# Kernel optimization log

Hardware: AMD Instinct MI355X
Metric: run time of the kernel (lower is better)

## Reference

```python
import jax, jax.numpy as jnp
import numpy as np

N, E = 100000, 1600000
IN_DIM, HID, NCLS = 64, 128, 18
BATCH, K = 8, 5000


def setup_inputs() -> dict:
    key = jax.random.key(0)
    ks = jax.random.split(key, 9)
    features = jax.random.normal(ks[0], (N, IN_DIM), dtype=jnp.float32)
    src = jax.random.randint(ks[1], (E,), 0, N, dtype=jnp.int32)
    dst = jax.random.randint(ks[2], (E,), 0, N, dtype=jnp.int32)
    def glorot(k, shape):
        lim = float(np.sqrt(6.0 / (shape[0] + shape[1])))
        return jax.random.uniform(k, shape, jnp.float32, -lim, lim)
    W1 = glorot(ks[3], (IN_DIM, HID)); b1 = jnp.zeros((HID,), jnp.float32)
    W2 = glorot(ks[4], (HID, HID));    b2 = jnp.zeros((HID,), jnp.float32)
    W3 = glorot(ks[5], (K * HID, NCLS)); b3 = jnp.zeros((NCLS,), jnp.float32)
    return {"features": features, "src": src, "dst": dst,
            "W1": W1, "b1": b1, "W2": W2, "b2": b2, "W3": W3, "b3": b3}


def reference(features, src, dst, W1, b1, W2, b2, W3, b3):
    n = features.shape[0]
    ones = jnp.ones(src.shape[0], features.dtype)
    out_deg = jax.ops.segment_sum(ones, src, num_segments=n)
    in_deg = jax.ops.segment_sum(ones, dst, num_segments=n)
    norm_src = jnp.clip(out_deg, 1.0) ** -0.5  # DGL norm='both'
    norm_dst = jnp.clip(in_deg, 1.0) ** -0.5

    def gconv(x, W, b, act):
        h = (x @ W) * norm_src[:, None]          # transform then normalize src
        agg = jax.ops.segment_sum(h[src], dst, num_segments=n)  # gather+scatter-add
        agg = agg * norm_dst[:, None] + b
        return jax.nn.relu(agg) if act else agg

    h = gconv(features, W1, b1, True)   # [N, HID]
    h = gconv(h, W2, b2, True)          # [N, HID]

    # global_sort_pool: equal-sized graphs of N//BATCH nodes, top-K by last channel
    n_per = n // BATCH
    hb = h.reshape(BATCH, n_per, HID)
    _, idx = jax.lax.top_k(hb[..., -1], K)                  # [B, K] descending
    topk = jnp.take_along_axis(hb, idx[..., None], axis=1)  # [B, K, HID]
    pooled = topk.reshape(BATCH, K * HID)

    return pooled @ W3 + b3  # [B, NCLS]
```

## Files before the change

### kernel.cpp

```cpp
#include <hip/hip_runtime.h>
#include <cstdint>
#include <cstddef>

#define N_NODES 100000
#define N_EDGES 1600000
#define IN_DIM  64
#define HID     128
#define NCLS    18
#define BATCH   8
#define TOPK    5000
#define NPER    12500
#define SORTN   16384
#define SORTC   2048

#define BSHIFT  9
#define BNODES  (1 << BSHIFT)
#define NBUCK   ((N_NODES + BNODES - 1) / BNODES)
#define CHUNK   8192


__global__ __launch_bounds__(256) void k_bcount(const int* __restrict__ src,
                                                const int* __restrict__ dst,
                                                int* __restrict__ bcntS,
                                                int* __restrict__ bcntD) {
    __shared__ int cs[NBUCK], cd[NBUCK];
    for (int b = threadIdx.x; b < NBUCK; b += 256) { cs[b] = 0; cd[b] = 0; }
    __syncthreads();
    const int base = blockIdx.x * CHUNK;
    const int end  = min(base + CHUNK, N_EDGES);
    for (int e = base + threadIdx.x; e < end; e += 256) {
        atomicAdd(&cs[src[e] >> BSHIFT], 1);
        atomicAdd(&cd[dst[e] >> BSHIFT], 1);
    }
    __syncthreads();
    for (int b = threadIdx.x; b < NBUCK; b += 256) {
        if (cs[b]) atomicAdd(&bcntS[b], cs[b]);
        if (cd[b]) atomicAdd(&bcntD[b], cd[b]);
    }
}

__global__ void k_bscan(const int* __restrict__ bcntS, const int* __restrict__ bcntD,
                        int* __restrict__ baseS, int* __restrict__ baseD,
                        int* __restrict__ curS, int* __restrict__ curD) {
    if (threadIdx.x == 0 && blockIdx.x == 0) {
        int rs = 0, rd = 0;
        for (int b = 0; b < NBUCK; ++b) {
            baseS[b] = rs; curS[b] = rs; rs += bcntS[b];
            baseD[b] = rd; curD[b] = rd; rd += bcntD[b];
        }
        baseS[NBUCK] = rs; baseD[NBUCK] = rd;
    }
}


__global__ __launch_bounds__(256) void k_bin2(const int* __restrict__ src,
                                              const int* __restrict__ dst,
                                              int* __restrict__ cursorD,
                                              int* __restrict__ cursorS,
                                              unsigned* __restrict__ binbuf,
                                              unsigned* __restrict__ sbin) {
    __shared__ int cD[NBUCK], gD[NBUCK], aD[NBUCK];
    __shared__ int cS[NBUCK], gS[NBUCK], aS[NBUCK];
    const int base = blockIdx.x * CHUNK;
    const int end  = min(base + CHUNK, N_EDGES);
    for (int b = threadIdx.x; b < NBUCK; b += 256) {
        cD[b] = 0; aD[b] = 0; cS[b] = 0; aS[b] = 0;
    }
    __syncthreads();
    for (int e = base + threadIdx.x; e < end; e += 256) {
        atomicAdd(&cD[dst[e] >> BSHIFT], 1);
        atomicAdd(&cS[src[e] >> BSHIFT], 1);
    }
    __syncthreads();
    for (int b = threadIdx.x; b < NBUCK; b += 256) {
        if (cD[b] > 0) gD[b] = atomicAdd(&cursorD[b], cD[b]);
        if (cS[b] > 0) gS[b] = atomicAdd(&cursorS[b], cS[b]);
    }
    __syncthreads();
    for (int e = base + threadIdx.x; e < end; e += 256) {
        int d = dst[e], s = src[e];
        int bd = d >> BSHIFT;
        int od = atomicAdd(&aD[bd], 1);
        binbuf[gD[bd] + od] = ((unsigned)(d & (BNODES - 1)) << 17) | (unsigned)s;
        int bs = s >> BSHIFT;
        int os = atomicAdd(&aS[bs], 1);
        sbin[gS[bs] + os] = (unsigned)(s & (BNODES - 1));
    }
}


__global__ __launch_bounds__(256) void k_hist_all(const unsigned* __restrict__ sbin,
                                                  const int* __restrict__ baseS,
                                                  const unsigned* __restrict__ binbuf,
                                                  const int* __restrict__ baseD,
                                                  float* __restrict__ normS,
                                                  float* __restrict__ normD,
                                                  int* __restrict__ row_ptr,
                                                  int* __restrict__ ssrc) {
    __shared__ int cnt[BNODES];
    __shared__ int tmp[BNODES];
    const int nodeBase = blockIdx.x << BSHIFT;
    for (int t = threadIdx.x; t < BNODES; t += 256) cnt[t] = 0;
    __syncthreads();
    {
        const int beg = baseS[blockIdx.x], end = baseS[blockIdx.x + 1];
        for (int e = beg + threadIdx.x; e < end; e += 256)
            atomicAdd(&cnt[sbin[e]], 1);
    }
    __syncthreads();
    for (int t = threadIdx.x; t < BNODES; t += 256) {
        int node = nodeBase + t;
        if (node < N_NODES)
            normS[node] = 1.0f / sqrtf((float)max(cnt[t], 1));
        cnt[t] = 0;
    }
    __syncthreads();
    const int beg = baseD[blockIdx.x], end = baseD[blockIdx.x + 1];
    for (int e = beg + threadIdx.x; e < end; e += 256)
        atomicAdd(&cnt[binbuf[e] >> 17], 1);
    __syncthreads();
    for (int t = threadIdx.x; t < BNODES; t += 256) {
        int node = nodeBase + t;
        if (node < N_NODES)
            normD[node] = 1.0f / sqrtf((float)max(cnt[t], 1));
    }
    for (int s = 1; s < BNODES; s <<= 1) {
        for (int t = threadIdx.x; t < BNODES; t += 256)
            tmp[t] = (t >= s) ? cnt[t - s] + cnt[t] : cnt[t];
        __syncthreads();
        for (int t = threadIdx.x; t < BNODES; t += 256) cnt[t] = tmp[t];
        __syncthreads();
    }
    for (int t = threadIdx.x; t < BNODES; t += 256) {
        int b = beg + ((t == 0) ? 0 : cnt[t - 1]);
        tmp[t] = b;
        int node = nodeBase + t;
        if (node < N_NODES) row_ptr[node] = b;
    }
    if (blockIdx.x == 0 && threadIdx.x == 0) row_ptr[N_NODES] = N_EDGES;
    __syncthreads();
    for (int e = beg + threadIdx.x; e < end; e += 256) {
        unsigned v = binbuf[e];
        int pos = atomicAdd(&tmp[v >> 17], 1);
        ssrc[pos] = (int)(v & 0x1FFFFu);
    }
}


#define BMT 64
#define BKT 32

__global__ __launch_bounds__(256) void k_fused1(const float* __restrict__ X,
                                                const int* __restrict__ row_ptr,
                                                const int* __restrict__ ssrc,
                                                const float* __restrict__ normS,
                                                const float* __restrict__ W,
                                                const float* __restrict__ normD,
                                                const float* __restrict__ bias,
                                                float* __restrict__ out) {
    __shared__ float xs[BMT][IN_DIM + 4];
    __shared__ float ws[BKT * HID];

    const int tid = threadIdx.x;
    const int rt = blockIdx.x * BMT;

    {
        constexpr int LPN = IN_DIM / 4;
        constexpr int NCH = 256 / LPN;
        const int w = tid / LPN;
        const int lane = tid % LPN;
        const float4* __restrict__ hv = (const float4*)X;
        #pragma unroll
        for (int c = 0; c < BMT / NCH; ++c) {
            const int row = c * NCH + w;
            const int node = rt + row;
            float4 a4 = make_float4(0.f, 0.f, 0.f, 0.f);
            if (node < N_NODES) {
                const int beg = row_ptr[node], end = row_ptr[node + 1];
                int e = beg;
                for (; e + 4 <= end; e += 4) {
                    int s0 = ssrc[e + 0], s1 = ssrc[e + 1], s2 = ssrc[e + 2], s3 = ssrc[e + 3];
                    float n0 = normS[s0], n1 = normS[s1], n2 = normS[s2], n3 = normS[s3];
                    float4 v0 = hv[(size_t)s0 * LPN + lane];
                    float4 v1 = hv[(size_t)s1 * LPN + lane];
                    float4 v2 = hv[(size_t)s2 * LPN + lane];
                    float4 v3 = hv[(size_t)s3 * LPN + lane];
                    a4.x += v0.x * n0; a4.y += v0.y * n0; a4.z += v0.z * n0; a4.w += v0.w * n0;
                    a4.x += v1.x * n1; a4.y += v1.y * n1; a4.z += v1.z * n1; a4.w += v1.w * n1;
                    a4.x += v2.x * n2; a4.y += v2.y * n2; a4.z += v2.z * n2; a4.w += v2.w * n2;
                    a4.x += v3.x * n3; a4.y += v3.y * n3; a4.z += v3.z * n3; a4.w += v3.w * n3;
                }
                for (; e < end; ++e) {
                    int s0 = ssrc[e];
                    float n0 = normS[s0];
                    float4 v0 = hv[(size_t)s0 * LPN + lane];
                    a4.x += v0.x * n0; a4.y += v0.y * n0; a4.z += v0.z * n0; a4.w += v0.w * n0;
                }
            }
            *(float4*)&xs[row][lane * 4] = a4;
        }
    }

    const int tx = tid & 31;
    const int ty = tid >> 5;
    const int col0 = tx * 4;
    const int row0 = ty * 8;

    float acc[8][4];
    #pragma unroll
    for (int r = 0; r < 8; ++r)
        #pragma unroll
        for (int c = 0; c < 4; ++c) acc[r][c] = 0.f;

    for (int k0 = 0; k0 < IN_DIM; k0 += BKT) {
        __syncthreads();
        {
            const float4* wsrc = (const float4*)(W + (size_t)k0 * HID);
            #pragma unroll
            for (int i = tid; i < BKT * HID / 4; i += 256)
                ((float4*)ws)[i] = wsrc[i];
        }
        __syncthreads();
        #pragma unroll 4
        for (int k = 0; k < BKT; ++k) {
            float4 b = *(const float4*)&ws[k * HID + col0];
            float a[8];
            #pragma unroll
            for (int r = 0; r < 8; ++r) a[r] = xs[row0 + r][k0 + k];
            #pragma unroll
            for (int r = 0; r < 8; ++r) {
                acc[r][0] += a[r] * b.x;
                acc[r][1] += a[r] * b.y;
                acc[r][2] += a[r] * b.z;
                acc[r][3] += a[r] * b.w;
            }
        }
    }

    const float4 bb = *(const float4*)(bias + col0);
    #pragma unroll
    for (int r = 0; r < 8; ++r) {
        int gr = rt + row0 + r;
        if (gr < N_NODES) {
            float nd = normD[gr];
            float4 o;
            o.x = fmaxf(acc[r][0] * nd + bb.x, 0.f);
            o.y = fmaxf(acc[r][1] * nd + bb.y, 0.f);
            o.z = fmaxf(acc[r][2] * nd + bb.z, 0.f);
            o.w = fmaxf(acc[r][3] * nd + bb.w, 0.f);
            float ns = normS[gr];
            o.x *= ns; o.y *= ns; o.z *= ns; o.w *= ns;
            *(float4*)(out + (size_t)gr * HID + col0) = o;
        }
    }
}


#define ACC4(A, V) { A.x += V.x; A.y += V.y; A.z += V.z; A.w += V.w; }

__global__ __launch_bounds__(256) void k_agg128(const float* __restrict__ hs,
                                                const int* __restrict__ row_ptr,
                                                const int* __restrict__ ssrc,
                                                float* __restrict__ out) {
    const int node = blockIdx.x * 8 + (threadIdx.x >> 5);
    const int lane = threadIdx.x & 31;
    if (node >= N_NODES) return;
    const int beg = row_ptr[node], end = row_ptr[node + 1];
    const float4* __restrict__ hv = (const float4*)hs;
    float4 acc = make_float4(0.f, 0.f, 0.f, 0.f);
    int e = beg;
    for (; e + 4 <= end; e += 4) {
        int s0 = ssrc[e + 0], s1 = ssrc[e + 1], s2 = ssrc[e + 2], s3 = ssrc[e + 3];
        float4 v0 = hv[(size_t)s0 * 32 + lane];
        float4 v1 = hv[(size_t)s1 * 32 + lane];
        float4 v2 = hv[(size_t)s2 * 32 + lane];
        float4 v3 = hv[(size_t)s3 * 32 + lane];
        ACC4(acc, v0); ACC4(acc, v1); ACC4(acc, v2); ACC4(acc, v3);
    }
    for (; e < end; ++e) {
        float4 v0 = hv[(size_t)ssrc[e] * 32 + lane];
        ACC4(acc, v0);
    }
    *(float4*)(out + (size_t)node * HID + lane * 4) = acc;
}


__global__ __launch_bounds__(256) void k_gemm2(const float* __restrict__ X,
                                               const float* __restrict__ W,
                                               const float* __restrict__ normD,
                                               const float* __restrict__ bias,
                                               float* __restrict__ keys,
                                               float* __restrict__ out) {
    __shared__ float xs[BMT][BKT + 4];
    __shared__ float ws[BKT * HID];

    const int tid = threadIdx.x;
    const int tx = tid & 31;
    const int ty = tid >> 5;
    const int col0 = tx * 4;
    const int row0 = ty * 8;
    const int rt = blockIdx.x * BMT;

    float acc[8][4];
    #pragma unroll
    for (int r = 0; r < 8; ++r)
        #pragma unroll
        for (int c = 0; c < 4; ++c) acc[r][c] = 0.f;

    for (int k0 = 0; k0 < HID; k0 += BKT) {
        __syncthreads();
        {
            const float4* wsrc = (const float4*)(W + (size_t)k0 * HID);
            #pragma unroll
            for (int i = tid; i < BKT * HID / 4; i += 256)
                ((float4*)ws)[i] = wsrc[i];
        }
        {
            #pragma unroll
            for (int i = tid; i < BMT * BKT / 4; i += 256) {
                int row = i >> 3;
                int kq  = i & 7;
                int gr  = rt + row;
                float4 v = make_float4(0.f, 0.f, 0.f, 0.f);
                if (gr < N_NODES)
                    v = *(const float4*)(X + (size_t)gr * HID + k0 + kq * 4);
                *(float4*)&xs[row][kq * 4] = v;
            }
        }
        __syncthreads();

        #pragma unroll 4
        for (int k = 0; k < BKT; ++k) {
            float4 b = *(const float4*)&ws[k * HID + col0];
            float a[8];
            #pragma unroll
            for (int r = 0; r < 8; ++r) a[r] = xs[row0 + r][k];
            #pragma unroll
            for (int r = 0; r < 8; ++r) {
                acc[r][0] += a[r] * b.x;
                acc[r][1] += a[r] * b.y;
                acc[r][2] += a[r] * b.z;
                acc[r][3] += a[r] * b.w;
            }
        }
    }

    const float4 bb = *(const float4*)(bias + col0);
    #pragma unroll
    for (int r = 0; r < 8; ++r) {
        int gr = rt + row0 + r;
        if (gr < N_NODES) {
            float nd = normD[gr];
            float4 o;
            o.x = fmaxf(acc[r][0] * nd + bb.x, 0.f);
            o.y = fmaxf(acc[r][1] * nd + bb.y, 0.f);
            o.z = fmaxf(acc[r][2] * nd + bb.z, 0.f);
            o.w = fmaxf(acc[r][3] * nd + bb.w, 0.f);
            if (col0 == 124) keys[gr] = o.w;
            *(float4*)(out + (size_t)gr * HID + col0) = o;
        }
    }
}


__global__ __launch_bounds__(256) void k_sort_init(const float* __restrict__ keys,
                                                   unsigned long long* __restrict__ arr) {
    int i = blockIdx.x * 256 + threadIdx.x;
    if (i >= BATCH * SORTN) return;
    int g = i >> 14;
    int l = i & (SORTN - 1);
    unsigned long long c;
    if (l < NPER) {
        unsigned u = __float_as_uint(keys[g * NPER + l]);
        unsigned s = (u & 0x80000000u) ? ~u : (u | 0x80000000u);
        unsigned d = ~s;
        c = ((unsigned long long)d << 32) | (unsigned)l;
    } else {
        c = 0xFFFFFFFFFFFFFFFFull;
    }
    arr[i] = c;
}

__global__ __launch_bounds__(1024) void k_sort_local_full(unsigned long long* __restrict__ arr) {
    __shared__ unsigned long long lds[SORTC];
    const int base  = blockIdx.x * SORTC;
    const int gbase = base & (SORTN - 1);
    lds[threadIdx.x]        = arr[base + threadIdx.x];
    lds[threadIdx.x + 1024] = arr[base + threadIdx.x + 1024];
    __syncthreads();
    for (int k = 2; k <= SORTC; k <<= 1) {
        for (int j = k >> 1; j > 0; j >>= 1) {
            int t = threadIdx.x;
            int i = ((t & ~(j - 1)) << 1) | (t & (j - 1));
            bool up = (((gbase + i) & k) == 0);
            unsigned long long a = lds[i], b = lds[i + j];
            if ((a > b) == up) { lds[i] = b; lds[i + j] = a; }
            __syncthreads();
        }
    }
    arr[base + threadIdx.x]        = lds[threadIdx.x];
    arr[base + threadIdx.x + 1024] = lds[threadIdx.x + 1024];
}

__global__ __launch_bounds__(256) void k_sort_global(unsigned long long* __restrict__ arr,
                                                     int k, int j) {
    int tg = blockIdx.x * 256 + threadIdx.x;
    if (tg >= BATCH * (SORTN / 2)) return;
    int g = tg >> 13;
    int t = tg & (SORTN / 2 - 1);
    int i = ((t & ~(j - 1)) << 1) | (t & (j - 1));
    bool up = ((i & k) == 0);
    unsigned long long* p = arr + (size_t)g * SORTN;
    unsigned long long a = p[i], b = p[i + j];
    if ((a > b) == up) { p[i] = b; p[i + j] = a; }
}

__global__ __launch_bounds__(1024) void k_sort_local_tail(unsigned long long* __restrict__ arr,
                                                          int k) {
    __shared__ unsigned long long lds[SORTC];
    const int base  = blockIdx.x * SORTC;
    const int gbase = base & (SORTN - 1);
    lds[threadIdx.x]        = arr[base + threadIdx.x];
    lds[threadIdx.x + 1024] = arr[base + threadIdx.x + 1024];
    __syncthreads();
    for (int j = SORTC >> 1; j > 0; j >>= 1) {
        int t = threadIdx.x;
        int i = ((t & ~(j - 1)) << 1) | (t & (j - 1));
        bool up = (((gbase + i) & k) == 0);
        unsigned long long a = lds[i], b = lds[i + j];
        if ((a > b) == up) { lds[i] = b; lds[i + j] = a; }
        __syncthreads();
    }
    arr[base + threadIdx.x]        = lds[threadIdx.x];
    arr[base + threadIdx.x + 1024] = lds[threadIdx.x + 1024];
}

__global__ __launch_bounds__(256) void k_sort_emit(const unsigned long long* __restrict__ arr,
                                                   int* __restrict__ topk_idx,
                                                   const float* __restrict__ b3,
                                                   float* __restrict__ out) {
    int i = blockIdx.x * 256 + threadIdx.x;
    if (i < BATCH * NCLS) out[i] = b3[i % NCLS];
    if (i >= BATCH * TOPK) return;
    int b = i / TOPK;
    int k = i - b * TOPK;
    topk_idx[i] = (int)(arr[(size_t)b * SORTN + k] & 0xFFFFFFFFull);
}


#define KPB 100

__global__ __launch_bounds__(128) void k_final(const float* __restrict__ h2,
                                               const int* __restrict__ topk_idx,
                                               const float* __restrict__ W3,
                                               float* __restrict__ out) {
    __shared__ float red[128 * NCLS];
    const int b = blockIdx.x / (TOPK / KPB);
    const int chunk = blockIdx.x % (TOPK / KPB);
    const int j = threadIdx.x;
    float acc[NCLS];
    #pragma unroll
    for (int c = 0; c < NCLS; ++c) acc[c] = 0.f;
    const int k0 = chunk * KPB;
    for (int k = k0; k < k0 + KPB; ++k) {
        int node = b * NPER + topk_idx[b * TOPK + k];
        float h = h2[(size_t)node * HID + j];
        const float* wrow = W3 + (size_t)(k * HID + j) * NCLS;
        #pragma unroll
        for (int c = 0; c < NCLS; ++c) acc[c] += h * wrow[c];
    }
    #pragma unroll
    for (int c = 0; c < NCLS; ++c) red[j * NCLS + c] = acc[c];
    __syncthreads();
    for (int s = 64; s > 0; s >>= 1) {
        if (j < s) {
            #pragma unroll
            for (int c = 0; c < NCLS; ++c) red[j * NCLS + c] += red[(j + s) * NCLS + c];
        }
        __syncthreads();
    }
    if (j < NCLS) atomicAdd(&out[b * NCLS + j], red[j]);
}


extern "C" void kernel_launch(void* const* d_in, const int* in_sizes, int n_in,
                              void* d_out, int out_size, void* d_ws, size_t ws_size,
                              hipStream_t stream) {
    const float* features = (const float*)d_in[0];
    const int*   src      = (const int*)d_in[1];
    const int*   dst      = (const int*)d_in[2];
    const float* W1       = (const float*)d_in[3];
    const float* b1       = (const float*)d_in[4];
    const float* W2       = (const float*)d_in[5];
    const float* b2       = (const float*)d_in[6];
    const float* W3       = (const float*)d_in[7];
    const float* b3       = (const float*)d_in[8];
    float* out = (float*)d_out;

    char* p = (char*)d_ws;
    auto carve = [&](size_t bytes) -> void* {
        void* r = (void*)p;
        p += (bytes + 511) & ~(size_t)511;
        return r;
    };
    float* normS     = (float*)carve((size_t)N_NODES * 4);
    float* normD     = (float*)carve((size_t)N_NODES * 4);
    int*   row_ptr   = (int*)carve((size_t)(N_NODES + 1) * 4);
    int*   bcntS     = (int*)carve((size_t)NBUCK * 4);
    int*   bcntD     = (int*)carve((size_t)NBUCK * 4);
    int*   baseS     = (int*)carve((size_t)(NBUCK + 1) * 4);
    int*   baseD     = (int*)carve((size_t)(NBUCK + 1) * 4);
    int*   curS      = (int*)carve((size_t)NBUCK * 4);
    int*   curD      = (int*)carve((size_t)NBUCK * 4);
    int*   ssrc      = (int*)carve((size_t)N_EDGES * 4);
    unsigned* binbuf = (unsigned*)carve((size_t)N_EDGES * 4);
    unsigned* sbin   = (unsigned*)carve((size_t)N_EDGES * 4);
    float* keys      = (float*)carve((size_t)N_NODES * 4);
    int*   topk_idx  = (int*)carve((size_t)BATCH * TOPK * 4);
    unsigned long long* sortbuf = (unsigned long long*)carve((size_t)BATCH * SORTN * 8);
    float* bufA      = (float*)carve((size_t)N_NODES * HID * 4);
    float* bufB      = (float*)carve((size_t)N_NODES * HID * 4);

    const int GB = (N_NODES + BMT - 1) / BMT;
    const int BB = (N_EDGES + CHUNK - 1) / CHUNK;

    hipMemsetAsync(bcntS, 0, (size_t)NBUCK * 4, stream);
    hipMemsetAsync(bcntD, 0, (size_t)NBUCK * 4, stream);

    k_bcount<<<BB, 256, 0, stream>>>(src, dst, bcntS, bcntD);
    k_bscan<<<1, 64, 0, stream>>>(bcntS, bcntD, baseS, baseD, curS, curD);
    k_bin2<<<BB, 256, 0, stream>>>(src, dst, curD, curS, binbuf, sbin);
    k_hist_all<<<NBUCK, 256, 0, stream>>>(sbin, baseS, binbuf, baseD,
                                          normS, normD, row_ptr, ssrc);

    k_fused1<<<GB, 256, 0, stream>>>(features, row_ptr, ssrc, normS, W1, normD, b1, bufA);
    k_agg128<<<(N_NODES + 7) / 8, 256, 0, stream>>>(bufA, row_ptr, ssrc, bufB);
    k_gemm2<<<GB, 256, 0, stream>>>(bufB, W2, normD, b2, keys, bufA);

    const int NCHUNK = BATCH * SORTN / SORTC;
    const int GCE    = (BATCH * (SORTN / 2) + 255) / 256;
    k_sort_init<<<(BATCH * SORTN + 255) / 256, 256, 0, stream>>>(keys, sortbuf);
    k_sort_local_full<<<NCHUNK, 1024, 0, stream>>>(sortbuf);
    k_sort_global<<<GCE, 256, 0, stream>>>(sortbuf, 4096, 2048);
    k_sort_local_tail<<<NCHUNK, 1024, 0, stream>>>(sortbuf, 4096);
    k_sort_global<<<GCE, 256, 0, stream>>>(sortbuf, 8192, 4096);
    k_sort_global<<<GCE, 256, 0, stream>>>(sortbuf, 8192, 2048);
    k_sort_local_tail<<<NCHUNK, 1024, 0, stream>>>(sortbuf, 8192);
    k_sort_global<<<GCE, 256, 0, stream>>>(sortbuf, 16384, 8192);
    k_sort_global<<<GCE, 256, 0, stream>>>(sortbuf, 16384, 4096);
    k_sort_global<<<GCE, 256, 0, stream>>>(sortbuf, 16384, 2048);
    k_sort_local_tail<<<NCHUNK, 1024, 0, stream>>>(sortbuf, 16384);
    k_sort_emit<<<(BATCH * TOPK + 255) / 256, 256, 0, stream>>>(sortbuf, topk_idx, b3, out);

    k_final<<<BATCH * (TOPK / KPB), 128, 0, stream>>>(bufA, topk_idx, W3, out);
}
```

Before: 578.4 us.

## Restructure bitonic top-k sort into fewer LDS-resident merge kernels

```diff
diff --git a/kernel.cpp b/kernel.cpp
--- a/kernel.cpp
+++ b/kernel.cpp
@@ -149,6 +149,7 @@
 
 #define BMT 64
 #define BKT 32
+#define BKT1 16
 
 __global__ __launch_bounds__(256) void k_fused1(const float* __restrict__ X,
                                                 const int* __restrict__ row_ptr,
@@ -159,7 +160,7 @@
                                                 const float* __restrict__ bias,
                                                 float* __restrict__ out) {
     __shared__ float xs[BMT][IN_DIM + 4];
-    __shared__ float ws[BKT * HID];
+    __shared__ float ws[BKT1 * HID];
 
     const int tid = threadIdx.x;
     const int rt = blockIdx.x * BMT;
@@ -212,17 +213,17 @@
         #pragma unroll
         for (int c = 0; c < 4; ++c) acc[r][c] = 0.f;
 
-    for (int k0 = 0; k0 < IN_DIM; k0 += BKT) {
+    for (int k0 = 0; k0 < IN_DIM; k0 += BKT1) {
         __syncthreads();
         {
             const float4* wsrc = (const float4*)(W + (size_t)k0 * HID);
             #pragma unroll
-            for (int i = tid; i < BKT * HID / 4; i += 256)
+            for (int i = tid; i < BKT1 * HID / 4; i += 256)
                 ((float4*)ws)[i] = wsrc[i];
         }
         __syncthreads();
         #pragma unroll 4
-        for (int k = 0; k < BKT; ++k) {
+        for (int k = 0; k < BKT1; ++k) {
             float4 b = *(const float4*)&ws[k * HID + col0];
             float a[8];
             #pragma unroll
@@ -363,30 +364,26 @@
 }
 
 
-__global__ __launch_bounds__(256) void k_sort_init(const float* __restrict__ keys,
-                                                   unsigned long long* __restrict__ arr) {
-    int i = blockIdx.x * 256 + threadIdx.x;
-    if (i >= BATCH * SORTN) return;
-    int g = i >> 14;
-    int l = i & (SORTN - 1);
-    unsigned long long c;
-    if (l < NPER) {
-        unsigned u = __float_as_uint(keys[g * NPER + l]);
-        unsigned s = (u & 0x80000000u) ? ~u : (u | 0x80000000u);
-        unsigned d = ~s;
-        c = ((unsigned long long)d << 32) | (unsigned)l;
-    } else {
-        c = 0xFFFFFFFFFFFFFFFFull;
-    }
-    arr[i] = c;
-}
-
-__global__ __launch_bounds__(1024) void k_sort_local_full(unsigned long long* __restrict__ arr) {
+__global__ __launch_bounds__(1024) void k_sort_local0(const float* __restrict__ keys,
+                                                      unsigned long long* __restrict__ arr) {
     __shared__ unsigned long long lds[SORTC];
     const int base  = blockIdx.x * SORTC;
     const int gbase = base & (SORTN - 1);
-    lds[threadIdx.x]        = arr[base + threadIdx.x];
-    lds[threadIdx.x + 1024] = arr[base + threadIdx.x + 1024];
+    for (int idx = threadIdx.x; idx < SORTC; idx += 1024) {
+        int gi = base + idx;
+        int g = gi >> 14;
+        int l = gi & (SORTN - 1);
+        unsigned long long c;
+        if (l < NPER) {
+            unsigned u = __float_as_uint(keys[g * NPER + l]);
+            unsigned s = (u & 0x80000000u) ? ~u : (u | 0x80000000u);
+            unsigned d = ~s;
+            c = ((unsigned long long)d << 32) | (unsigned)l;
+        } else {
+            c = 0xFFFFFFFFFFFFFFFFull;
+        }
+        lds[idx] = c;
+    }
     __syncthreads();
     for (int k = 2; k <= SORTC; k <<= 1) {
         for (int j = k >> 1; j > 0; j >>= 1) {
@@ -402,49 +399,45 @@
     arr[base + threadIdx.x + 1024] = lds[threadIdx.x + 1024];
 }
 
-__global__ __launch_bounds__(256) void k_sort_global(unsigned long long* __restrict__ arr,
-                                                     int k, int j) {
-    int tg = blockIdx.x * 256 + threadIdx.x;
-    if (tg >= BATCH * (SORTN / 2)) return;
-    int g = tg >> 13;
-    int t = tg & (SORTN / 2 - 1);
-    int i = ((t & ~(j - 1)) << 1) | (t & (j - 1));
-    bool up = ((i & k) == 0);
-    unsigned long long* p = arr + (size_t)g * SORTN;
-    unsigned long long a = p[i], b = p[i + j];
-    if ((a > b) == up) { p[i] = b; p[i + j] = a; }
-}
-
-__global__ __launch_bounds__(1024) void k_sort_local_tail(unsigned long long* __restrict__ arr,
-                                                          int k) {
-    __shared__ unsigned long long lds[SORTC];
-    const int base  = blockIdx.x * SORTC;
+template<int SPAN>
+__global__ __launch_bounds__(1024) void k_sort_span(unsigned long long* __restrict__ arr) {
+    __shared__ unsigned long long lds[SPAN];
+    const int base  = blockIdx.x * SPAN;
     const int gbase = base & (SORTN - 1);
-    lds[threadIdx.x]        = arr[base + threadIdx.x];
-    lds[threadIdx.x + 1024] = arr[base + threadIdx.x + 1024];
-    __syncthreads();
-    for (int j = SORTC >> 1; j > 0; j >>= 1) {
-        int t = threadIdx.x;
-        int i = ((t & ~(j - 1)) << 1) | (t & (j - 1));
-        bool up = (((gbase + i) & k) == 0);
-        unsigned long long a = lds[i], b = lds[i + j];
-        if ((a > b) == up) { lds[i] = b; lds[i + j] = a; }
-        __syncthreads();
-    }
-    arr[base + threadIdx.x]        = lds[threadIdx.x];
-    arr[base + threadIdx.x + 1024] = lds[threadIdx.x + 1024];
-}
-
-__global__ __launch_bounds__(256) void k_sort_emit(const unsigned long long* __restrict__ arr,
-                                                   int* __restrict__ topk_idx,
-                                                   const float* __restrict__ b3,
-                                                   float* __restrict__ out) {
-    int i = blockIdx.x * 256 + threadIdx.x;
-    if (i < BATCH * NCLS) out[i] = b3[i % NCLS];
-    if (i >= BATCH * TOPK) return;
-    int b = i / TOPK;
-    int k = i - b * TOPK;
-    topk_idx[i] = (int)(arr[(size_t)b * SORTN + k] & 0xFFFFFFFFull);
+    const bool up = ((gbase / SPAN) & 1) == 0;
+    for (int i = threadIdx.x; i < SPAN; i += 1024) lds[i] = arr[base + i];
+    __syncthreads();
+    for (int j = SPAN >> 1; j > 0; j >>= 1) {
+        for (int t = threadIdx.x; t < SPAN / 2; t += 1024) {
+            int i = ((t & ~(j - 1)) << 1) | (t & (j - 1));
+            unsigned long long a = lds[i], b = lds[i + j];
+            if ((a > b) == up) { lds[i] = b; lds[i + j] = a; }
+        }
+        __syncthreads();
+    }
+    for (int i = threadIdx.x; i < SPAN; i += 1024) arr[base + i] = lds[i];
+}
+
+__global__ __launch_bounds__(1024) void k_sort_final16k(const unsigned long long* __restrict__ arr,
+                                                        int* __restrict__ topk_idx,
+                                                        const float* __restrict__ b3,
+                                                        float* __restrict__ out) {
+    __shared__ unsigned long long lds[SORTN];
+    const int base = blockIdx.x * SORTN;
+    for (int i = threadIdx.x; i < SORTN; i += 1024) lds[i] = arr[base + i];
+    __syncthreads();
+    for (int j = SORTN >> 1; j > 0; j >>= 1) {
+        for (int t = threadIdx.x; t < SORTN / 2; t += 1024) {
+            int i = ((t & ~(j - 1)) << 1) | (t & (j - 1));
+            unsigned long long a = lds[i], b = lds[i + j];
+            if (a > b) { lds[i] = b; lds[i + j] = a; }
+        }
+        __syncthreads();
+    }
+    for (int i = threadIdx.x; i < TOPK; i += 1024)
+        topk_idx[blockIdx.x * TOPK + i] = (int)(lds[i] & 0xFFFFFFFFull);
+    if (blockIdx.x == 0 && threadIdx.x < BATCH * NCLS)
+        out[threadIdx.x] = b3[threadIdx.x % NCLS];
 }
 
 
@@ -537,20 +530,10 @@
     k_agg128<<<(N_NODES + 7) / 8, 256, 0, stream>>>(bufA, row_ptr, ssrc, bufB);
     k_gemm2<<<GB, 256, 0, stream>>>(bufB, W2, normD, b2, keys, bufA);
 
-    const int NCHUNK = BATCH * SORTN / SORTC;
-    const int GCE    = (BATCH * (SORTN / 2) + 255) / 256;
-    k_sort_init<<<(BATCH * SORTN + 255) / 256, 256, 0, stream>>>(keys, sortbuf);
-    k_sort_local_full<<<NCHUNK, 1024, 0, stream>>>(sortbuf);
-    k_sort_global<<<GCE, 256, 0, stream>>>(sortbuf, 4096, 2048);
-    k_sort_local_tail<<<NCHUNK, 1024, 0, stream>>>(sortbuf, 4096);
-    k_sort_global<<<GCE, 256, 0, stream>>>(sortbuf, 8192, 4096);
-    k_sort_global<<<GCE, 256, 0, stream>>>(sortbuf, 8192, 2048);
-    k_sort_local_tail<<<NCHUNK, 1024, 0, stream>>>(sortbuf, 8192);
-    k_sort_global<<<GCE, 256, 0, stream>>>(sortbuf, 16384, 8192);
-    k_sort_global<<<GCE, 256, 0, stream>>>(sortbuf, 16384, 4096);
-    k_sort_global<<<GCE, 256, 0, stream>>>(sortbuf, 16384, 2048);
-    k_sort_local_tail<<<NCHUNK, 1024, 0, stream>>>(sortbuf, 16384);
-    k_sort_emit<<<(BATCH * TOPK + 255) / 256, 256, 0, stream>>>(sortbuf, topk_idx, b3, out);
+    k_sort_local0<<<BATCH * SORTN / SORTC, 1024, 0, stream>>>(keys, sortbuf);
+    k_sort_span<4096><<<BATCH * SORTN / 4096, 1024, 0, stream>>>(sortbuf);
+    k_sort_span<8192><<<BATCH * SORTN / 8192, 1024, 0, stream>>>(sortbuf);
+    k_sort_final16k<<<BATCH, 1024, 0, stream>>>(sortbuf, topk_idx, b3, out);
 
     k_final<<<BATCH * (TOPK / KPB), 128, 0, stream>>>(bufA, topk_idx, W3, out);
 }
```

Measured after the change: 594.6 us. 2.8% more time.
